# Kernel optimization log

Measured on AMD Instinct MI355X. Metric: run time of the kernel, lower is better.

Reference implementation:

```python
import jax, jax.numpy as jnp
import numpy as np

B, S, H, NH = 4, 2048, 1024, 16
DK = H // NH

def setup_inputs() -> dict:
    key = jax.random.key(0)
    ks = jax.random.split(key, 8)
    query = jax.random.normal(ks[0], (B, S, H), dtype=jnp.float32)
    key_t = jax.random.normal(ks[1], (B, S, H), dtype=jnp.float32)
    value = jax.random.normal(ks[2], (B, S, H), dtype=jnp.float32)
    mask = jnp.ones((B, S), dtype=jnp.int32)
    # Linear weights (torch convention: y = x @ W.T + b)
    sc = 1.0 / np.sqrt(H)
    Wq = jax.random.uniform(ks[3], (H, H), jnp.float32, -sc, sc)
    Wk = jax.random.uniform(ks[4], (H, H), jnp.float32, -sc, sc)
    Wv = jax.random.uniform(ks[5], (H, H), jnp.float32, -sc, sc)
    Wo = jax.random.uniform(ks[6], (H, H), jnp.float32, -sc, sc)
    bo = jax.random.uniform(ks[7], (H,), jnp.float32, -sc, sc)
    return {"query": query, "key": key_t, "value": value, "mask": mask,
            "Wq": Wq, "Wk": Wk, "Wv": Wv, "Wo": Wo, "bo": bo}

def reference(query, key, value, mask, Wq, Wk, Wv, Wo, bo):
    # project and split heads: (B,S,H) -> (B,NH,S,DK)
    def split_heads(x, W):
        y = x @ W.T
        return y.reshape(B, S, NH, DK).transpose(0, 2, 1, 3)
    q = split_heads(query, Wq)
    k = split_heads(key, Wk)
    v = split_heads(value, Wv)
    scores = jnp.einsum('bhqd,bhkd->bhqk', q, k) / jnp.sqrt(jnp.float32(DK))
    # outer-product padding mask: (B,S)x(B,S) -> (B,1,S,S)
    m = (mask[:, :, None] * mask[:, None, :])[:, None, :, :]
    scores = jnp.where(m == 0, jnp.float32(-1e9), scores)
    p = jax.nn.softmax(scores, axis=-1)  # dropout off (eval mode)
    x = jnp.einsum('bhqk,bhkd->bhqd', p, v)
    x = x.transpose(0, 2, 1, 3).reshape(B, S, H)
    return x @ Wo.T + bo
```

## Files before the change

kernel.cpp:

```cpp
#include <hip/hip_runtime.h>

typedef unsigned short u16;
typedef __bf16 bf16x8 __attribute__((ext_vector_type(8)));
typedef __bf16 bf16x4 __attribute__((ext_vector_type(4)));
typedef float f32x4 __attribute__((ext_vector_type(4)));

#if __has_builtin(__builtin_amdgcn_exp2f)
#define EXP2(x) __builtin_amdgcn_exp2f(x)
#else
#define EXP2(x) exp2f(x)
#endif

__device__ __forceinline__ u16 f2bf(float f) {
    unsigned u = __float_as_uint(f);
    u += 0x7fffu + ((u >> 16) & 1u);
    return (u16)(u >> 16);
}

__device__ __forceinline__ void gll16(const void* g, void* l) {
    __builtin_amdgcn_global_load_lds(
        (const __attribute__((address_space(1))) void*)g,
        (__attribute__((address_space(3))) void*)l, 16, 0, 0);
}

__device__ __forceinline__ void cvt_body(const float* __restrict__ in,
                                         u16* __restrict__ out, int i) {
    float4 v = reinterpret_cast<const float4*>(in)[i];
    unsigned long long pack =
        (unsigned long long)f2bf(v.x) |
        ((unsigned long long)f2bf(v.y) << 16) |
        ((unsigned long long)f2bf(v.z) << 32) |
        ((unsigned long long)f2bf(v.w) << 48);
    reinterpret_cast<unsigned long long*>(out)[i] = pack;
}

__global__ __launch_bounds__(256) void cvt_all(const float* __restrict__ q,
                                               const float* __restrict__ k,
                                               const float* __restrict__ v,
                                               const float* __restrict__ wq,
                                               const float* __restrict__ wk,
                                               const float* __restrict__ wv,
                                               const float* __restrict__ wo,
                                               u16* __restrict__ oq,
                                               u16* __restrict__ ok,
                                               u16* __restrict__ ov,
                                               u16* __restrict__ owq,
                                               u16* __restrict__ owk,
                                               u16* __restrict__ owv,
                                               u16* __restrict__ owo,
                                               int n4, int nw4) {
    int i = blockIdx.x * 256 + threadIdx.x;
    if (i < n4)          cvt_body(q, oq, i);
    else if (i < 2 * n4) cvt_body(k, ok, i - n4);
    else if (i < 3 * n4) cvt_body(v, ov, i - 2 * n4);
    else {
        int j = i - 3 * n4;
        if (j < nw4)          cvt_body(wq, owq, j);
        else if (j < 2 * nw4) cvt_body(wk, owk, j - nw4);
        else if (j < 3 * nw4) cvt_body(wv, owv, j - 2 * nw4);
        else if (j < 4 * nw4) cvt_body(wo, owo, j - 3 * nw4);
    }
}

template<int MODE>
__global__ __launch_bounds__(256) void gemm_bt(const u16* __restrict__ A,
                                               const u16* __restrict__ B,
                                               void* __restrict__ Cv,
                                               const float* __restrict__ bias) {
    constexpr int K = 1024, N = 1024;
    __shared__ __align__(16) u16 As[128 * 64];
    __shared__ __align__(16) u16 Bs[128 * 64];
    const int tid = threadIdx.x;
    const int wv = tid >> 6, lane = tid & 63, g = lane >> 4, li = lane & 15;
    const int row0 = blockIdx.y << 7, col0 = blockIdx.x << 7;
    const int wm = wv >> 1, wn = wv & 1;

    f32x4 acc[4][4] = {};

    for (int k0 = 0; k0 < K; k0 += 64) {
        __syncthreads();
#pragma unroll
        for (int i = 0; i < 4; i++) {
            const int o   = (wv << 12) + (i << 10) + (lane << 4);
            const int row = o >> 7;
            const int cbg = (o & 127) ^ ((row & 7) << 4);
            gll16(A + (size_t)(row0 + row) * K + k0 + (cbg >> 1),
                  (char*)As + (wv << 12) + (i << 10));
        }
#pragma unroll
        for (int i = 0; i < 4; i++) {
            const int o   = (wv << 12) + (i << 10) + (lane << 4);
            const int row = o >> 7;
            const int cbg = (o & 127) ^ ((row & 7) << 4);
            gll16(B + (size_t)(col0 + row) * K + k0 + (cbg >> 1),
                  (char*)Bs + (wv << 12) + (i << 10));
        }
        __syncthreads();

#pragma unroll
        for (int kk = 0; kk < 2; kk++) {
            bf16x8 af[4], bfr[4];
            const int cb = ((kk << 5) + (g << 3)) << 1;
#pragma unroll
            for (int m = 0; m < 4; m++) {
                const int row = (wm << 6) + (m << 4) + li;
                af[m] = *reinterpret_cast<const bf16x8*>(
                    (const char*)As + (row << 7) + (cb ^ ((row & 7) << 4)));
            }
#pragma unroll
            for (int n = 0; n < 4; n++) {
                const int row = (wn << 6) + (n << 4) + li;
                bfr[n] = *reinterpret_cast<const bf16x8*>(
                    (const char*)Bs + (row << 7) + (cb ^ ((row & 7) << 4)));
            }
#pragma unroll
            for (int m = 0; m < 4; m++)
#pragma unroll
                for (int n = 0; n < 4; n++)
                    acc[m][n] = __builtin_amdgcn_mfma_f32_16x16x32_bf16(
                        af[m], bfr[n], acc[m][n], 0, 0, 0);
        }
    }

    if constexpr (MODE == 0 || MODE == 3) {
        constexpr float SC = (MODE == 3) ? 0.180336880f : 1.0f;
        u16* C = (u16*)Cv;
#pragma unroll
        for (int m = 0; m < 4; m++)
#pragma unroll
            for (int n = 0; n < 4; n++)
#pragma unroll
                for (int r = 0; r < 4; r++) {
                    int row = row0 + (wm << 6) + (m << 4) + (g << 2) + r;
                    int col = col0 + (wn << 6) + (n << 4) + li;
                    C[(size_t)row * N + col] = f2bf(acc[m][n][r] * SC);
                }
    } else if constexpr (MODE == 1) {
        float* C = (float*)Cv;
#pragma unroll
        for (int m = 0; m < 4; m++)
#pragma unroll
            for (int n = 0; n < 4; n++)
#pragma unroll
                for (int r = 0; r < 4; r++) {
                    int row = row0 + (wm << 6) + (m << 4) + (g << 2) + r;
                    int col = col0 + (wn << 6) + (n << 4) + li;
                    C[(size_t)row * N + col] = acc[m][n][r] + bias[col];
                }
    } else {
        u16* C = (u16*)Cv;
#pragma unroll
        for (int m = 0; m < 4; m++)
#pragma unroll
            for (int n = 0; n < 4; n++) {
                int srow = row0 + (wm << 6) + (m << 4) + (g << 2);
                int col  = col0 + (wn << 6) + (n << 4) + li;
                int b = srow >> 11, s = srow & 2047;
                int nh = col >> 6, d = col & 63;
                unsigned long long pack =
                    (unsigned long long)f2bf(acc[m][n][0]) |
                    ((unsigned long long)f2bf(acc[m][n][1]) << 16) |
                    ((unsigned long long)f2bf(acc[m][n][2]) << 32) |
                    ((unsigned long long)f2bf(acc[m][n][3]) << 48);
                *reinterpret_cast<unsigned long long*>(
                    C + ((size_t)((b << 4) + nh) * 64 + d) * 2048 + s) = pack;
            }
    }
}

__global__ __launch_bounds__(512, 4) void attn_fwd(const u16* __restrict__ Q,
                                                   const u16* __restrict__ Kp,
                                                   const u16* __restrict__ Vt,
                                                   const int* __restrict__ mask,
                                                   u16* __restrict__ O) {
    constexpr int S = 2048, H = 1024;
    constexpr int K0OFF = 0, K1OFF = 8192, V0OFF = 16384, V1OFF = 24576;
    __shared__ __align__(16) char lds[32768];
    __shared__ int sm_bad;
    const int tid = threadIdx.x, wv = tid >> 6, lane = tid & 63;
    const int g = lane >> 4, li = lane & 15;
    const int q0 = blockIdx.x << 7, h = blockIdx.y, b = blockIdx.z;
    const char* Kg = (const char*)(Kp + (size_t)b * S * H + h * 64);
    const char* Vg = (const char*)(Vt + (size_t)(b * 16 + h) * 64 * S);

    auto stageK = [&](int koff, int kv2) {
        const int o   = tid << 4;
        const int row = o >> 7;
        const int cbg = (o & 127) ^ ((row & 7) << 4);
        const int gk  = (((row >> 2) & 3) << 4) + ((row >> 4) << 2) + (row & 3);
        gll16(Kg + (size_t)(kv2 + gk) * 2048 + cbg, lds + koff + (wv << 10));
    };
    auto stageV = [&](int voff, int kv2) {
        const int o   = tid << 4;
        const int row = o >> 7;
        const int cbg = (o & 127) ^ ((row & 7) << 4);
        gll16(Vg + (size_t)row * 4096 + kv2 * 2 + cbg, lds + voff + (wv << 10));
    };

    if (tid == 0) sm_bad = 0;
    stageK(K0OFF, 0);
    stageV(V0OFF, 0);
    stageK(K1OFF, 64);

    bf16x8 qf[2];
    {
        const u16* Qrow = Q + (size_t)(b * S + q0 + (wv << 4) + li) * H + h * 64 + (g << 3);
        qf[0] = *reinterpret_cast<const bf16x8*>(Qrow);
        qf[1] = *reinterpret_cast<const bf16x8*>(Qrow + 32);
    }

    int z = 0;
#pragma unroll
    for (int j = 0; j < 4; j++) z |= (mask[b * S + (tid << 2) + j] == 0);
    __syncthreads();
    if (z) sm_bad = 1;

    int offK[2], offV[2];
#pragma unroll
    for (int kk = 0; kk < 2; kk++) {
        offK[kk] = (li << 7) + (((kk << 6) + (g << 4)) ^ ((li & 7) << 4));
        offV[kk] = (li << 7) + (((g << 5) + (kk << 4)) ^ ((li & 7) << 4));
    }

    f32x4 scE[4] = {}, scO[4] = {};
    auto QK = [&](int koff, f32x4 (&sc)[4]) {
#pragma unroll
        for (int n = 0; n < 4; n++) sc[n] = f32x4{};
        __builtin_amdgcn_s_setprio(1);
#pragma unroll
        for (int kk = 0; kk < 2; kk++)
#pragma unroll
            for (int n = 0; n < 4; n++) {
                bf16x8 kf = *reinterpret_cast<const bf16x8*>(
                    lds + koff + offK[kk] + (n << 11));
                sc[n] = __builtin_amdgcn_mfma_f32_16x16x32_bf16(kf, qf[kk], sc[n], 0, 0, 0);
            }
        __builtin_amdgcn_s_setprio(0);
    };

    QK(K0OFF, scE);
    __syncthreads();
    const bool bad = (sm_bad != 0);
    const int  mq  = bad ? mask[b * S + q0 + (wv << 4) + li] : 1;

    f32x4 o_[4] = {};
    float l_ = 0.f;
    bf16x8 pfE[2], pfO[2];

    auto SM = [&](f32x4 (&sc)[4], bf16x8 (&pf)[2], int kv2) {
        if (bad) {
            const unsigned long long kb = __ballot(mask[b * S + kv2 + lane] != 0);
#pragma unroll
            for (int n = 0; n < 4; n++)
#pragma unroll
                for (int r = 0; r < 4; r++) {
                    const int key = (g << 4) + (n << 2) + r;
                    const bool ok = mq && ((kb >> key) & 1ull);
                    sc[n][r] = ok ? sc[n][r] : -1e9f;
                }
        }
        float rs = 0.f;
#pragma unroll
        for (int n = 0; n < 4; n++)
#pragma unroll
            for (int r = 0; r < 4; r++) {
                const float p = EXP2(sc[n][r]);
                sc[n][r] = p;
                rs += p;
            }
        rs += __shfl_xor(rs, 16);
        rs += __shfl_xor(rs, 32);
        l_ += rs;
#pragma unroll
        for (int j = 0; j < 4; j++) {
            pf[0][j]     = (__bf16)sc[0][j];
            pf[0][4 + j] = (__bf16)sc[1][j];
            pf[1][j]     = (__bf16)sc[2][j];
            pf[1][4 + j] = (__bf16)sc[3][j];
        }
    };

    auto PV = [&](int voff, bf16x8 (&pf)[2]) {
        __builtin_amdgcn_s_setprio(1);
#pragma unroll
        for (int kk = 0; kk < 2; kk++)
#pragma unroll
            for (int n = 0; n < 4; n++) {
                bf16x8 vf = *reinterpret_cast<const bf16x8*>(
                    lds + voff + offV[kk] + (n << 11));
                o_[n] = __builtin_amdgcn_mfma_f32_16x16x32_bf16(pf[kk], vf, o_[n], 0, 0, 0);
            }
        __builtin_amdgcn_s_setprio(0);
    };

    for (int kv = 0; kv < S; kv += 128) {
        stageV(V1OFF, kv + 64);
        QK(K1OFF, scO);
        if (kv + 128 < S) stageK(K0OFF, kv + 128);
        SM(scE, pfE, kv);
        PV(V0OFF, pfE);
        __syncthreads();
        if (kv + 128 < S) {
            stageV(V0OFF, kv + 128);
            QK(K0OFF, scE);
        }
        if (kv + 192 < S) stageK(K1OFF, kv + 192);
        SM(scO, pfO, kv + 64);
        PV(V1OFF, pfO);
        __syncthreads();
    }

    float linv[4];
#pragma unroll
    for (int r = 0; r < 4; r++) {
        const float lr = __shfl(l_, (lane & 48) + (g << 2) + r);
        linv[r] = lr > 0.f ? 1.f / lr : 0.f;
    }
#pragma unroll
    for (int n = 0; n < 4; n++)
#pragma unroll
        for (int r = 0; r < 4; r++) {
            const int row = q0 + (wv << 4) + (g << 2) + r;
            const int col = (h << 6) + (n << 4) + li;
            O[(size_t)(b * S + row) * H + col] = f2bf(o_[n][r] * linv[r]);
        }
}

extern "C" void kernel_launch(void* const* d_in, const int* in_sizes, int n_in,
                              void* d_out, int out_size, void* d_ws, size_t ws_size,
                              hipStream_t stream) {
    (void)in_sizes; (void)n_in; (void)out_size; (void)ws_size;
    const float* q    = (const float*)d_in[0];
    const float* k    = (const float*)d_in[1];
    const float* v    = (const float*)d_in[2];
    const int*   mask = (const int*)d_in[3];
    const float* Wq   = (const float*)d_in[4];
    const float* Wk   = (const float*)d_in[5];
    const float* Wv   = (const float*)d_in[6];
    const float* Wo   = (const float*)d_in[7];
    const float* bo   = (const float*)d_in[8];

    const size_t NEL = 8192ull * 1024ull;
    u16* ws  = (u16*)d_ws;
    u16* r0  = ws;
    u16* r1  = ws + NEL;
    u16* r2  = ws + 2 * NEL;
    u16* wqb = ws + 3 * NEL;
    u16* wkb = wqb + 1024 * 1024;
    u16* wvb = wkb + 1024 * 1024;
    u16* wob = wvb + 1024 * 1024;
    u16* r4  = wob + 1024 * 1024;

    const int n4  = (int)(NEL / 4);
    const int nw4 = 262144;
    const int cvt_blocks = (3 * n4 + 4 * nw4 + 255) / 256;
    cvt_all<<<dim3(cvt_blocks), dim3(256), 0, stream>>>(
        q, k, v, Wq, Wk, Wv, Wo, r0, r1, r2, wqb, wkb, wvb, wob, n4, nw4);

    dim3 gg(8, 64), bb(256);
    gemm_bt<3><<<gg, bb, 0, stream>>>(r0, wqb, r4, nullptr);
    gemm_bt<0><<<gg, bb, 0, stream>>>(r1, wkb, r0, nullptr);
    gemm_bt<2><<<gg, bb, 0, stream>>>(r2, wvb, r1, nullptr);

    attn_fwd<<<dim3(16, 16, 4), dim3(512), 0, stream>>>(r4, r0, r1, mask, r2);

    gemm_bt<1><<<gg, bb, 0, stream>>>(r2, wob, d_out, bo);
}
```

Baseline: 219.1 us.

## Fuse fp32-to-bf16 activation conversion into batched QKV projection and swizzle attention grid

Activations are no longer converted to bf16 in a separate pass. The QKV projection kernel now reads fp32 directly, converts the values in registers and writes them to LDS, and all three projections run in one launch using a z grid dimension. The conversion kernel now handles only the weights. The attention grid is flattened and block indices are swizzled, which changes which heads and batches run at the same time and may improve K/V cache reuse. The cost is a synchronous global-to-register load path in the QKV GEMM, replacing the async global-to-LDS loads, and it reads twice as many bytes per A tile.

```diff
diff --git a/kernel.cpp b/kernel.cpp
--- a/kernel.cpp
+++ b/kernel.cpp
@@ -2,7 +2,6 @@
 
 typedef unsigned short u16;
 typedef __bf16 bf16x8 __attribute__((ext_vector_type(8)));
-typedef __bf16 bf16x4 __attribute__((ext_vector_type(4)));
 typedef float f32x4 __attribute__((ext_vector_type(4)));
 
 #if __has_builtin(__builtin_amdgcn_exp2f)
@@ -34,39 +33,30 @@
     reinterpret_cast<unsigned long long*>(out)[i] = pack;
 }
 
-__global__ __launch_bounds__(256) void cvt_all(const float* __restrict__ q,
-                                               const float* __restrict__ k,
-                                               const float* __restrict__ v,
-                                               const float* __restrict__ wq,
-                                               const float* __restrict__ wk,
-                                               const float* __restrict__ wv,
-                                               const float* __restrict__ wo,
-                                               u16* __restrict__ oq,
-                                               u16* __restrict__ ok,
-                                               u16* __restrict__ ov,
-                                               u16* __restrict__ owq,
-                                               u16* __restrict__ owk,
-                                               u16* __restrict__ owv,
-                                               u16* __restrict__ owo,
-                                               int n4, int nw4) {
+__global__ __launch_bounds__(256) void cvt_w(const float* __restrict__ a,
+                                             const float* __restrict__ b,
+                                             const float* __restrict__ c,
+                                             const float* __restrict__ d,
+                                             u16* __restrict__ oa,
+                                             u16* __restrict__ ob,
+                                             u16* __restrict__ oc,
+                                             u16* __restrict__ od, int n4) {
     int i = blockIdx.x * 256 + threadIdx.x;
-    if (i < n4)          cvt_body(q, oq, i);
-    else if (i < 2 * n4) cvt_body(k, ok, i - n4);
-    else if (i < 3 * n4) cvt_body(v, ov, i - 2 * n4);
-    else {
-        int j = i - 3 * n4;
-        if (j < nw4)          cvt_body(wq, owq, j);
-        else if (j < 2 * nw4) cvt_body(wk, owk, j - nw4);
-        else if (j < 3 * nw4) cvt_body(wv, owv, j - 2 * nw4);
-        else if (j < 4 * nw4) cvt_body(wo, owo, j - 3 * nw4);
-    }
-}
-
-template<int MODE>
-__global__ __launch_bounds__(256) void gemm_bt(const u16* __restrict__ A,
-                                               const u16* __restrict__ B,
-                                               void* __restrict__ Cv,
-                                               const float* __restrict__ bias) {
+    if (i < n4)            cvt_body(a, oa, i);
+    else if (i < 2 * n4)   cvt_body(b, ob, i - n4);
+    else if (i < 3 * n4)   cvt_body(c, oc, i - 2 * n4);
+    else if (i < 4 * n4)   cvt_body(d, od, i - 3 * n4);
+}
+
+__global__ __launch_bounds__(256) void qkv_proj(const float* __restrict__ Aq,
+                                                const float* __restrict__ Ak,
+                                                const float* __restrict__ Av,
+                                                const u16* __restrict__ Bq,
+                                                const u16* __restrict__ Bk,
+                                                const u16* __restrict__ Bv,
+                                                u16* __restrict__ Cq,
+                                                u16* __restrict__ Ck,
+                                                u16* __restrict__ Cv) {
     constexpr int K = 1024, N = 1024;
     __shared__ __align__(16) u16 As[128 * 64];
     __shared__ __align__(16) u16 Bs[128 * 64];
@@ -74,18 +64,36 @@
     const int wv = tid >> 6, lane = tid & 63, g = lane >> 4, li = lane & 15;
     const int row0 = blockIdx.y << 7, col0 = blockIdx.x << 7;
     const int wm = wv >> 1, wn = wv & 1;
+    const int zm = blockIdx.z;
+    const float* A32 = zm == 0 ? Aq : zm == 1 ? Ak : Av;
+    const u16*   B   = zm == 0 ? Bq : zm == 1 ? Bk : Bv;
+    u16*         C   = zm == 0 ? Cq : zm == 1 ? Ck : Cv;
 
     f32x4 acc[4][4] = {};
 
     for (int k0 = 0; k0 < K; k0 += 64) {
-        __syncthreads();
+        float4 la[4][2];
 #pragma unroll
         for (int i = 0; i < 4; i++) {
             const int o   = (wv << 12) + (i << 10) + (lane << 4);
             const int row = o >> 7;
             const int cbg = (o & 127) ^ ((row & 7) << 4);
-            gll16(A + (size_t)(row0 + row) * K + k0 + (cbg >> 1),
-                  (char*)As + (wv << 12) + (i << 10));
+            const float4* src = reinterpret_cast<const float4*>(
+                A32 + (size_t)(row0 + row) * K + k0 + (cbg >> 1));
+            la[i][0] = src[0];
+            la[i][1] = src[1];
+        }
+        __syncthreads();
+#pragma unroll
+        for (int i = 0; i < 4; i++) {
+            const int o = (wv << 12) + (i << 10) + (lane << 4);
+            bf16x8 t;
+#pragma unroll
+            for (int j = 0; j < 4; j++) {
+                t[j]     = (__bf16)la[i][0][j];
+                t[4 + j] = (__bf16)la[i][1][j];
+            }
+            *reinterpret_cast<bf16x8*>((char*)As + o) = t;
         }
 #pragma unroll
         for (int i = 0; i < 4; i++) {
@@ -122,33 +130,7 @@
         }
     }
 
-    if constexpr (MODE == 0 || MODE == 3) {
-        constexpr float SC = (MODE == 3) ? 0.180336880f : 1.0f;
-        u16* C = (u16*)Cv;
-#pragma unroll
-        for (int m = 0; m < 4; m++)
-#pragma unroll
-            for (int n = 0; n < 4; n++)
-#pragma unroll
-                for (int r = 0; r < 4; r++) {
-                    int row = row0 + (wm << 6) + (m << 4) + (g << 2) + r;
-                    int col = col0 + (wn << 6) + (n << 4) + li;
-                    C[(size_t)row * N + col] = f2bf(acc[m][n][r] * SC);
-                }
-    } else if constexpr (MODE == 1) {
-        float* C = (float*)Cv;
-#pragma unroll
-        for (int m = 0; m < 4; m++)
-#pragma unroll
-            for (int n = 0; n < 4; n++)
-#pragma unroll
-                for (int r = 0; r < 4; r++) {
-                    int row = row0 + (wm << 6) + (m << 4) + (g << 2) + r;
-                    int col = col0 + (wn << 6) + (n << 4) + li;
-                    C[(size_t)row * N + col] = acc[m][n][r] + bias[col];
-                }
-    } else {
-        u16* C = (u16*)Cv;
+    if (zm == 2) {
 #pragma unroll
         for (int m = 0; m < 4; m++)
 #pragma unroll
@@ -165,7 +147,90 @@
                 *reinterpret_cast<unsigned long long*>(
                     C + ((size_t)((b << 4) + nh) * 64 + d) * 2048 + s) = pack;
             }
-    }
+    } else {
+        const float SC = zm == 0 ? 0.180336880f : 1.0f;
+#pragma unroll
+        for (int m = 0; m < 4; m++)
+#pragma unroll
+            for (int n = 0; n < 4; n++)
+#pragma unroll
+                for (int r = 0; r < 4; r++) {
+                    int row = row0 + (wm << 6) + (m << 4) + (g << 2) + r;
+                    int col = col0 + (wn << 6) + (n << 4) + li;
+                    C[(size_t)row * N + col] = f2bf(acc[m][n][r] * SC);
+                }
+    }
+}
+
+__global__ __launch_bounds__(256) void out_proj(const u16* __restrict__ A,
+                                                const u16* __restrict__ B,
+                                                float* __restrict__ C,
+                                                const float* __restrict__ bias) {
+    constexpr int K = 1024, N = 1024;
+    __shared__ __align__(16) u16 As[128 * 64];
+    __shared__ __align__(16) u16 Bs[128 * 64];
+    const int tid = threadIdx.x;
+    const int wv = tid >> 6, lane = tid & 63, g = lane >> 4, li = lane & 15;
+    const int row0 = blockIdx.y << 7, col0 = blockIdx.x << 7;
+    const int wm = wv >> 1, wn = wv & 1;
+
+    f32x4 acc[4][4] = {};
+
+    for (int k0 = 0; k0 < K; k0 += 64) {
+        __syncthreads();
+#pragma unroll
+        for (int i = 0; i < 4; i++) {
+            const int o   = (wv << 12) + (i << 10) + (lane << 4);
+            const int row = o >> 7;
+            const int cbg = (o & 127) ^ ((row & 7) << 4);
+            gll16(A + (size_t)(row0 + row) * K + k0 + (cbg >> 1),
+                  (char*)As + (wv << 12) + (i << 10));
+        }
+#pragma unroll
+        for (int i = 0; i < 4; i++) {
+            const int o   = (wv << 12) + (i << 10) + (lane << 4);
+            const int row = o >> 7;
+            const int cbg = (o & 127) ^ ((row & 7) << 4);
+            gll16(B + (size_t)(col0 + row) * K + k0 + (cbg >> 1),
+                  (char*)Bs + (wv << 12) + (i << 10));
+        }
+        __syncthreads();
+
+#pragma unroll
+        for (int kk = 0; kk < 2; kk++) {
+            bf16x8 af[4], bfr[4];
+            const int cb = ((kk << 5) + (g << 3)) << 1;
+#pragma unroll
+            for (int m = 0; m < 4; m++) {
+                const int row = (wm << 6) + (m << 4) + li;
+                af[m] = *reinterpret_cast<const bf16x8*>(
+                    (const char*)As + (row << 7) + (cb ^ ((row & 7) << 4)));
+            }
+#pragma unroll
+            for (int n = 0; n < 4; n++) {
+                const int row = (wn << 6) + (n << 4) + li;
+                bfr[n] = *reinterpret_cast<const bf16x8*>(
+                    (const char*)Bs + (row << 7) + (cb ^ ((row & 7) << 4)));
+            }
+#pragma unroll
+            for (int m = 0; m < 4; m++)
+#pragma unroll
+                for (int n = 0; n < 4; n++)
+                    acc[m][n] = __builtin_amdgcn_mfma_f32_16x16x32_bf16(
+                        af[m], bfr[n], acc[m][n], 0, 0, 0);
+        }
+    }
+
+#pragma unroll
+    for (int m = 0; m < 4; m++)
+#pragma unroll
+        for (int n = 0; n < 4; n++)
+#pragma unroll
+            for (int r = 0; r < 4; r++) {
+                int row = row0 + (wm << 6) + (m << 4) + (g << 2) + r;
+                int col = col0 + (wn << 6) + (n << 4) + li;
+                C[(size_t)row * N + col] = acc[m][n][r] + bias[col];
+            }
 }
 
 __global__ __launch_bounds__(512, 4) void attn_fwd(const u16* __restrict__ Q,
@@ -179,7 +244,9 @@
     __shared__ int sm_bad;
     const int tid = threadIdx.x, wv = tid >> 6, lane = tid & 63;
     const int g = lane >> 4, li = lane & 15;
-    const int q0 = blockIdx.x << 7, h = blockIdx.y, b = blockIdx.z;
+    const int bid = blockIdx.x;
+    const int swz = ((bid & 7) << 7) + (bid >> 3);
+    const int q0 = (swz & 15) << 7, h = (swz >> 4) & 15, b = swz >> 8;
     const char* Kg = (const char*)(Kp + (size_t)b * S * H + h * 64);
     const char* Vg = (const char*)(Vt + (size_t)(b * 16 + h) * 64 * S);
 
@@ -351,18 +418,13 @@
     u16* wob = wvb + 1024 * 1024;
     u16* r4  = wob + 1024 * 1024;
 
-    const int n4  = (int)(NEL / 4);
-    const int nw4 = 262144;
-    const int cvt_blocks = (3 * n4 + 4 * nw4 + 255) / 256;
-    cvt_all<<<dim3(cvt_blocks), dim3(256), 0, stream>>>(
-        q, k, v, Wq, Wk, Wv, Wo, r0, r1, r2, wqb, wkb, wvb, wob, n4, nw4);
-
-    dim3 gg(8, 64), bb(256);
-    gemm_bt<3><<<gg, bb, 0, stream>>>(r0, wqb, r4, nullptr);
-    gemm_bt<0><<<gg, bb, 0, stream>>>(r1, wkb, r0, nullptr);
-    gemm_bt<2><<<gg, bb, 0, stream>>>(r2, wvb, r1, nullptr);
-
-    attn_fwd<<<dim3(16, 16, 4), dim3(512), 0, stream>>>(r4, r0, r1, mask, r2);
-
-    gemm_bt<1><<<gg, bb, 0, stream>>>(r2, wob, d_out, bo);
-}
+    cvt_w<<<dim3(4096), dim3(256), 0, stream>>>(Wq, Wk, Wv, Wo,
+                                                wqb, wkb, wvb, wob, 262144);
+
+    qkv_proj<<<dim3(8, 64, 3), dim3(256), 0, stream>>>(
+        q, k, v, wqb, wkb, wvb, r4, r0, r1);
+
+    attn_fwd<<<dim3(1024), dim3(512), 0, stream>>>(r4, r0, r1, mask, r2);
+
+    out_proj<<<dim3(8, 64), dim3(256), 0, stream>>>(r2, wob, (float*)d_out, bo);
+}
```

After: 237.2 us. 1.08x slower.
